# Kernel optimization log

Hardware: AMD Instinct MI355X
Metric: run time of the kernel (lower is better)

## Reference

```python
import jax, jax.numpy as jnp
import numpy as np

H = 2048          # hidden_size
I = 768           # moe_intermediate_size
E = 64            # num_experts
TOP_K = 8         # num_experts_per_tok (norm_topk_prob=True)
B, S = 1, 1024


def setup_inputs() -> dict:
    key = jax.random.key(0)
    ks = jax.random.split(key, 5)
    scale = 0.02
    return {
        "hidden_states": jax.random.normal(ks[0], (B, S, H), dtype=jnp.float32),
        "W_router": jax.random.normal(ks[1], (H, E), dtype=jnp.float32) * scale,
        "W_gate": jax.random.normal(ks[2], (E, H, I), dtype=jnp.float32) * scale,
        "W_up": jax.random.normal(ks[3], (E, H, I), dtype=jnp.float32) * scale,
        "W_down": jax.random.normal(ks[4], (E, I, H), dtype=jnp.float32) * scale,
    }


def reference(hidden_states, W_router, W_gate, W_up, W_down):
    b, s, h = hidden_states.shape
    x = hidden_states.reshape(-1, h)                      # [T, H]

    # --- Qwen3MoeTopKRouter: linear gate -> fp32 softmax -> top-k -> renorm ---
    logits = x @ W_router                                 # [T, E]
    probs = jax.nn.softmax(logits.astype(jnp.float32), axis=-1)
    top_w, top_idx = jax.lax.top_k(probs, TOP_K)          # [T, K]
    top_w = top_w / jnp.sum(top_w, axis=-1, keepdims=True)  # norm_topk_prob
    top_w = top_w.astype(x.dtype)

    # combine weights per (token, expert): zero if expert not selected
    comb = jnp.sum(jax.nn.one_hot(top_idx, E, dtype=x.dtype) * top_w[..., None], axis=1)  # [T, E]

    # --- per-expert SwiGLU MLP: down(silu(gate(x)) * up(x)), dense-masked ---
    g = jnp.einsum('th,ehi->eti', x, W_gate)              # [E, T, I]
    u = jnp.einsum('th,ehi->eti', x, W_up)                # [E, T, I]
    hmid = jax.nn.silu(g) * u                             # [E, T, I]
    # fold combine weight into the intermediate to avoid an [E, T, H] buffer
    hmid = hmid * comb.T[:, :, None]                      # [E, T, I]
    out = jnp.einsum('eti,eih->th', hmid, W_down)         # [T, H]

    return out.reshape(b, s, h)
```

## Files before the change

### kernel.cpp

```cpp
#include <hip/hip_runtime.h>
#include <hip/hip_bf16.h>

#define H_DIM 2048
#define I_DIM 768
#define NEXP 64
#define TOPK 8
#define NTOK 1024
#define BM 256
#define BKS 32

typedef float f32x4 __attribute__((ext_vector_type(4)));
typedef unsigned int u32x4 __attribute__((ext_vector_type(4)));
typedef unsigned int u32x2 __attribute__((ext_vector_type(2)));
typedef short bf16v8 __attribute__((ext_vector_type(8)));
typedef unsigned short u16x8 __attribute__((ext_vector_type(8)));
typedef unsigned int u32;

#define NTLOAD __builtin_nontemporal_load

#define WS_NEEDED 50954752ull

__device__ inline unsigned short f2bf(float f) {
    union { float f; u32 u; } v; v.f = f;
    u32 r = (v.u + 0x7FFFu + ((v.u >> 16) & 1u)) >> 16;
    return (unsigned short)r;
}
__device__ inline u32 pack2(float a, float b) {
    return (u32)f2bf(a) | ((u32)f2bf(b) << 16);
}

__global__ void zero_kernel(float4* p, int n4) {
    int i = blockIdx.x * blockDim.x + threadIdx.x;
    if (i < n4) p[i] = (float4){0.f, 0.f, 0.f, 0.f};
}

__global__ void xconv_kernel(const float4* __restrict__ x, ushort4* __restrict__ xbf, int n4) {
    int i = blockIdx.x * blockDim.x + threadIdx.x;
    if (i < n4) {
        float4 v = x[i];
        ushort4 o;
        o.x = f2bf(v.x); o.y = f2bf(v.y); o.z = f2bf(v.z); o.w = f2bf(v.w);
        xbf[i] = o;
    }
}

__global__ __launch_bounds__(256) void router_kernel(
    const float* __restrict__ x, const float* __restrict__ Wr,
    int* __restrict__ topk_idx, float* __restrict__ topk_w)
{
    const int t   = blockIdx.x;
    const int tid = threadIdx.x;
    const int lane = tid & 63;
    const int wv   = tid >> 6;
    __shared__ float xs[H_DIM];
    __shared__ float red[4][64];

    const float* xrow = x + (size_t)t * H_DIM;
    {
        const float4* src = (const float4*)xrow;
        float4* dst = (float4*)xs;
        dst[tid]       = src[tid];
        dst[tid + 256] = src[tid + 256];
    }
    __syncthreads();

    float acc = 0.f;
    const int h0 = wv * 512;
    #pragma unroll 8
    for (int h = h0; h < h0 + 512; ++h) acc += xs[h] * Wr[(size_t)h * NEXP + lane];
    red[wv][lane] = acc;
    __syncthreads();

    if (tid < 64) {
        const int e = tid;
        float logit = red[0][e] + red[1][e] + red[2][e] + red[3][e];

        float m = logit;
        #pragma unroll
        for (int o = 32; o > 0; o >>= 1) m = fmaxf(m, __shfl_xor(m, o));
        float p = __expf(logit - m);
        float s = p;
        #pragma unroll
        for (int o = 32; o > 0; o >>= 1) s += __shfl_xor(s, o);
        float prob = p / s;

        float myp = prob;
        float kw[TOPK]; int kid[TOPK]; float wsum = 0.f;
        #pragma unroll
        for (int k = 0; k < TOPK; ++k) {
            float v = myp; int bi = e;
            #pragma unroll
            for (int o = 32; o > 0; o >>= 1) {
                float ov = __shfl_xor(v, o);
                int   oi = __shfl_xor(bi, o);
                if (ov > v || (ov == v && oi < bi)) { v = ov; bi = oi; }
            }
            kw[k] = v; kid[k] = bi; wsum += v;
            if (e == bi) myp = -1.f;
        }
        if (e == 0) {
            float inv = 1.f / wsum;
            #pragma unroll
            for (int k = 0; k < TOPK; ++k) {
                topk_idx[t * TOPK + k] = kid[k];
                topk_w[t * TOPK + k]   = kw[k] * inv;
            }
        }
    }
}

__global__ __launch_bounds__(64) void listbuild_kernel(
    const int* __restrict__ topk_idx, const float* __restrict__ topk_w,
    int* __restrict__ counts, int* __restrict__ lists, float* __restrict__ wlist,
    int* __restrict__ invmap)
{
    const int e = blockIdx.x;
    const int lane = threadIdx.x;
    int n = 0;
    for (int base = 0; base < NTOK * TOPK; base += 64) {
        int s = base + lane;
        int idx = topk_idx[s];
        bool match = (idx == e);
        unsigned long long mask = __ballot(match);
        int pre = __popcll(mask & ((1ull << lane) - 1ull));
        if (match) {
            lists[e * NTOK + n + pre] = s >> 3;
            wlist[e * NTOK + n + pre] = topk_w[s];
            invmap[s] = n + pre;
        }
        n += __popcll(mask);
    }
    if (lane == 0) counts[e] = n;
}

__global__ __launch_bounds__(64) void scan_kernel(
    const int* __restrict__ counts, int* __restrict__ offsets)
{
    int e = threadIdx.x;
    int v = counts[e];
    int xacc = v;
    #pragma unroll
    for (int o = 1; o < 64; o <<= 1) {
        int y = __shfl_up(xacc, o);
        if (e >= o) xacc += y;
    }
    offsets[e] = xacc - v;
}

#define MFMA_BF16 __builtin_amdgcn_mfma_f32_16x16x32_bf16
#define LGKM0()  asm volatile("s_waitcnt lgkmcnt(0)" ::: "memory")
#define RAWBAR() __builtin_amdgcn_s_barrier()

__global__ __launch_bounds__(512) void gateup_kernel(
    const unsigned short* __restrict__ xbf,
    const float* __restrict__ Wg, const float* __restrict__ Wu,
    const int* __restrict__ counts, const int* __restrict__ offsets,
    const int* __restrict__ lists, const float* __restrict__ wlist,
    unsigned short* __restrict__ hmid)
{
    const int b  = blockIdx.x;
    const int wg = (b & 7) * 192 + (b >> 3);
    const int itile = wg % 24;
    const int e     = wg / 24;

    const int count = counts[e];
    if (count == 0) return;
    const int off = offsets[e];
    const int i0 = itile * 32;

    __shared__ unsigned short Alds[2][BM][40];
    __shared__ u32 Bgl[2][32 * 20];
    __shared__ u32 Bul[2][32 * 20];

    const int tid  = threadIdx.x;
    const int lane = tid & 63;
    const int wid  = tid >> 6;
    const int wm   = wid >> 1, wn = wid & 1;
    const int kb   = lane >> 4;
    const int l15  = lane & 15;

    const int ar = tid >> 1;
    const int ah = (tid & 1) * 16;
    const int bnn  = tid & 31;
    const int bkq  = (tid >> 5) & 7;
    const int bmat = tid >> 8;
    const float* WB = (bmat ? Wu : Wg) + (size_t)e * H_DIM * I_DIM + i0 + bnn;
    const int key4w = 4 * ((bnn >> 3) & 3);
    const int bwoff = bnn * 20 + ((2 * bkq) ^ key4w);
    const int brn   = wn * 16 + l15;
    const int key4r = 4 * ((brn >> 3) & 3);

    for (int mstart = 0; mstart < count; mstart += BM) {
        const int pr = mstart + ar;
        const bool aact = pr < count;
        const unsigned short* xrow = xbf + (size_t)(aact ? lists[e * NTOK + pr] : 0) * H_DIM + ah;
        const bool mact = (mstart + wm * 64) < count;

        f32x4 accg[4], accu[4];
        #pragma unroll
        for (int i = 0; i < 4; ++i) {
            accg[i] = (f32x4){0.f, 0.f, 0.f, 0.f};
            accu[i] = (f32x4){0.f, 0.f, 0.f, 0.f};
        }

        u32x4 aA0, aA1, aB0, aB1;
        float bA0, bA1, bA2, bA3;
        float bB0, bB1, bB2, bB3;

#define GU_LOADA(P0,P1,h)                                                       \
        if (aact) {                                                             \
            const u32x4* pa_ = (const u32x4*)(xrow + (h));                      \
            P0 = pa_[0]; P1 = pa_[1];                                           \
        }
#define GU_LOADB(R0,R1,R2,R3,h)                                                 \
        {                                                                       \
            R0 = NTLOAD(WB + (size_t)((h) + 4 * bkq)     * I_DIM);              \
            R1 = NTLOAD(WB + (size_t)((h) + 4 * bkq + 1) * I_DIM);              \
            R2 = NTLOAD(WB + (size_t)((h) + 4 * bkq + 2) * I_DIM);              \
            R3 = NTLOAD(WB + (size_t)((h) + 4 * bkq + 3) * I_DIM);              \
        }
#define GU_STORE(BUF,P0,P1,R0,R1,R2,R3)                                         \
        if (aact) {                                                             \
            *(u32x4*)&Alds[BUF][ar][ah]     = P0;                               \
            *(u32x4*)&Alds[BUF][ar][ah + 8] = P1;                               \
        }                                                                       \
        {                                                                       \
            u32x2 w_; w_.x = pack2(R0, R1); w_.y = pack2(R2, R3);               \
            *(u32x2*)((bmat ? Bul[BUF] : Bgl[BUF]) + bwoff) = w_;               \
        }
#define GU_MFMA(BUF)                                                            \
        if (mact) {                                                             \
            bf16v8 af[4], bg, bu;                                               \
            _Pragma("unroll")                                                   \
            for (int mf = 0; mf < 4; ++mf)                                      \
                af[mf] = *(const bf16v8*)&Alds[BUF][wm * 64 + mf * 16 + l15][kb * 8]; \
            bg = *(const bf16v8*)&Bgl[BUF][brn * 20 + ((4 * kb) ^ key4r)];      \
            bu = *(const bf16v8*)&Bul[BUF][brn * 20 + ((4 * kb) ^ key4r)];      \
            _Pragma("unroll")                                                   \
            for (int mf = 0; mf < 4; ++mf) {                                    \
                accg[mf] = MFMA_BF16(af[mf], bg, accg[mf], 0, 0, 0);            \
                accu[mf] = MFMA_BF16(af[mf], bu, accu[mf], 0, 0, 0);            \
            }                                                                   \
        }
#define GU_PHASE(BUF,P0,P1,R0,R1,R2,R3,nh)                                      \
        GU_STORE(BUF, P0, P1, R0, R1, R2, R3);                                  \
        if ((nh) < H_DIM) { GU_LOADB(R0, R1, R2, R3, (nh)); GU_LOADA(P0, P1, (nh)); } \
        LGKM0();                                                                \
        RAWBAR();                                                               \
        __builtin_amdgcn_s_setprio(1);                                          \
        GU_MFMA(BUF);                                                           \
        __builtin_amdgcn_s_setprio(0);

        GU_LOADB(bA0, bA1, bA2, bA3, 0);    GU_LOADA(aA0, aA1, 0);
        GU_LOADB(bB0, bB1, bB2, bB3, BKS);  GU_LOADA(aB0, aB1, BKS);

        for (int hh = 0; hh < H_DIM; hh += 2 * BKS) {
            GU_PHASE(0, aA0, aA1, bA0, bA1, bA2, bA3, hh + 2 * BKS);
            GU_PHASE(1, aB0, aB1, bB0, bB1, bB2, bB3, hh + 3 * BKS);
        }
        __syncthreads();
#undef GU_LOADA
#undef GU_LOADB
#undef GU_STORE
#undef GU_MFMA
#undef GU_PHASE

        if (mact) {
            #pragma unroll
            for (int mf = 0; mf < 4; ++mf)
                #pragma unroll
                for (int r = 0; r < 4; ++r) {
                    int pos = mstart + wm * 64 + mf * 16 + kb * 4 + r;
                    if (pos < count) {
                        float wgt = wlist[e * NTOK + pos];
                        float g = accg[mf][r], u = accu[mf][r];
                        float s = 1.f / (1.f + __expf(-g));
                        hmid[(size_t)(off + pos) * I_DIM + i0 + wn * 16 + l15] = f2bf(g * s * u * wgt);
                    }
                }
        }
    }
}

template <bool USE_PART>
__global__ __launch_bounds__(512) void down_kernel(
    const unsigned short* __restrict__ hmid, const float* __restrict__ Wd,
    const int* __restrict__ counts, const int* __restrict__ offsets,
    const int* __restrict__ lists, float* __restrict__ out,
    unsigned short* __restrict__ part)
{
    const int b  = blockIdx.x;
    const int wg = (b & 7) * 512 + (b >> 3);
    const int htile = wg % 64;
    const int e     = wg / 64;

    const int count = counts[e];
    if (count == 0) return;
    const int off = offsets[e];
    const int h0 = htile * 32;

    __shared__ unsigned short Alds[2][BM][40];
    __shared__ u32 Bdl[2][32 * 20];

    const int tid  = threadIdx.x;
    const int lane = tid & 63;
    const int wid  = tid >> 6;
    const int wm   = wid >> 1, wn = wid & 1;
    const int kb   = lane >> 4;
    const int l15  = lane & 15;

    const int ar = tid >> 1;
    const int ah = (tid & 1) * 16;
    const int bnn  = tid & 31;
    const int bkq  = (tid >> 5) & 7;
    const bool bact = tid < 256;
    const float* WB = Wd + (size_t)e * I_DIM * H_DIM + h0 + bnn;
    const int key4w = 4 * ((bnn >> 3) & 3);
    const int bwoff = bnn * 20 + ((2 * bkq) ^ key4w);
    const int brn   = wn * 16 + l15;
    const int key4r = 4 * ((brn >> 3) & 3);

    for (int mstart = 0; mstart < count; mstart += BM) {
        const int pr = mstart + ar;
        const bool aact = pr < count;
        const unsigned short* hrow = hmid + (size_t)(off + (aact ? pr : 0)) * I_DIM + ah;
        const bool mact = (mstart + wm * 64) < count;

        f32x4 acc[4];
        #pragma unroll
        for (int i = 0; i < 4; ++i) acc[i] = (f32x4){0.f, 0.f, 0.f, 0.f};

        u32x4 aA0, aA1, aB0, aB1;
        float bA0, bA1, bA2, bA3;
        float bB0, bB1, bB2, bB3;

#define DN_LOADA(P0,P1,k)                                                       \
        if (aact) {                                                             \
            const u32x4* p_ = (const u32x4*)(hrow + (k));                       \
            P0 = p_[0]; P1 = p_[1];                                             \
        }
#define DN_LOADB(R0,R1,R2,R3,k)                                                 \
        if (bact) {                                                             \
            R0 = NTLOAD(WB + (size_t)((k) + 4 * bkq)     * H_DIM);              \
            R1 = NTLOAD(WB + (size_t)((k) + 4 * bkq + 1) * H_DIM);              \
            R2 = NTLOAD(WB + (size_t)((k) + 4 * bkq + 2) * H_DIM);              \
            R3 = NTLOAD(WB + (size_t)((k) + 4 * bkq + 3) * H_DIM);              \
        }
#define DN_STORE(BUF,P0,P1,R0,R1,R2,R3)                                         \
        if (aact) {                                                             \
            *(u32x4*)&Alds[BUF][ar][ah]     = P0;                               \
            *(u32x4*)&Alds[BUF][ar][ah + 8] = P1;                               \
        }                                                                       \
        if (bact) {                                                             \
            u32x2 w_; w_.x = pack2(R0, R1); w_.y = pack2(R2, R3);               \
            *(u32x2*)(Bdl[BUF] + bwoff) = w_;                                   \
        }
#define DN_MFMA(BUF)                                                            \
        if (mact) {                                                             \
            bf16v8 af[4], bd;                                                   \
            _Pragma("unroll")                                                   \
            for (int mf = 0; mf < 4; ++mf)                                      \
                af[mf] = *(const bf16v8*)&Alds[BUF][wm * 64 + mf * 16 + l15][kb * 8]; \
            bd = *(const bf16v8*)&Bdl[BUF][brn * 20 + ((4 * kb) ^ key4r)];      \
            _Pragma("unroll")                                                   \
            for (int mf = 0; mf < 4; ++mf)                                      \
                acc[mf] = MFMA_BF16(af[mf], bd, acc[mf], 0, 0, 0);              \
        }
#define DN_PHASE(BUF,P0,P1,R0,R1,R2,R3,nk)                                      \
        DN_STORE(BUF, P0, P1, R0, R1, R2, R3);                                  \
        if ((nk) < I_DIM) { DN_LOADB(R0, R1, R2, R3, (nk)); DN_LOADA(P0, P1, (nk)); } \
        LGKM0();                                                                \
        RAWBAR();                                                               \
        __builtin_amdgcn_s_setprio(1);                                          \
        DN_MFMA(BUF);                                                           \
        __builtin_amdgcn_s_setprio(0);

        DN_LOADB(bA0, bA1, bA2, bA3, 0);    DN_LOADA(aA0, aA1, 0);
        DN_LOADB(bB0, bB1, bB2, bB3, BKS);  DN_LOADA(aB0, aB1, BKS);

        for (int ii = 0; ii < I_DIM; ii += 2 * BKS) {
            DN_PHASE(0, aA0, aA1, bA0, bA1, bA2, bA3, ii + 2 * BKS);
            DN_PHASE(1, aB0, aB1, bB0, bB1, bB2, bB3, ii + 3 * BKS);
        }
        __syncthreads();
#undef DN_LOADA
#undef DN_LOADB
#undef DN_STORE
#undef DN_MFMA
#undef DN_PHASE

        if (mact) {
            #pragma unroll
            for (int mf = 0; mf < 4; ++mf)
                #pragma unroll
                for (int r = 0; r < 4; ++r) {
                    int pos = mstart + wm * 64 + mf * 16 + kb * 4 + r;
                    if (pos < count) {
                        if constexpr (USE_PART) {
                            part[(size_t)(off + pos) * H_DIM + h0 + wn * 16 + l15] =
                                f2bf(acc[mf][r]);
                        } else {
                            int tok = lists[e * NTOK + pos];
                            atomicAdd(&out[(size_t)tok * H_DIM + h0 + wn * 16 + l15],
                                      acc[mf][r]);
                        }
                    }
                }
        }
    }
}

__global__ __launch_bounds__(256) void reduce_kernel(
    const unsigned short* __restrict__ part,
    const int* __restrict__ topk_idx, const int* __restrict__ invmap,
    const int* __restrict__ offsets, float* __restrict__ out)
{
    const int t   = blockIdx.x;
    const int tid = threadIdx.x;
    __shared__ int slots[TOPK];
    if (tid < TOPK) {
        int s = t * TOPK + tid;
        slots[tid] = offsets[topk_idx[s]] + invmap[s];
    }
    __syncthreads();

    const int c = tid * 8;
    float acc[8] = {0.f, 0.f, 0.f, 0.f, 0.f, 0.f, 0.f, 0.f};
    #pragma unroll
    for (int k = 0; k < TOPK; ++k) {
        u16x8 v = *(const u16x8*)&part[(size_t)slots[k] * H_DIM + c];
        #pragma unroll
        for (int j = 0; j < 8; ++j)
            acc[j] += __uint_as_float((u32)(unsigned short)v[j] << 16);
    }
    float4* dst = (float4*)&out[(size_t)t * H_DIM + c];
    dst[0] = (float4){acc[0], acc[1], acc[2], acc[3]};
    dst[1] = (float4){acc[4], acc[5], acc[6], acc[7]};
}

extern "C" void kernel_launch(void* const* d_in, const int* in_sizes, int n_in,
                              void* d_out, int out_size, void* d_ws, size_t ws_size,
                              hipStream_t stream) {
    const float* x  = (const float*)d_in[0];
    const float* Wr = (const float*)d_in[1];
    const float* Wg = (const float*)d_in[2];
    const float* Wu = (const float*)d_in[3];
    const float* Wd = (const float*)d_in[4];
    float* out = (float*)d_out;

    char* ws = (char*)d_ws;
    int*   topk_idx = (int*)  (ws + 0);
    float* topk_w   = (float*)(ws + 32768);
    int*   counts   = (int*)  (ws + 65536);
    int*   offsets  = (int*)  (ws + 65792);
    int*   lists    = (int*)  (ws + 66048);
    float* wlist    = (float*)(ws + 328192);
    int*   invmap   = (int*)  (ws + 590336);
    unsigned short* hmid = (unsigned short*)(ws + 623104);
    unsigned short* xbf  = (unsigned short*)(ws + 13206016);
    unsigned short* part = (unsigned short*)(ws + 17400320);

    const bool usePart = ws_size >= WS_NEEDED;

    hipLaunchKernelGGL(xconv_kernel, dim3((NTOK * H_DIM / 4 + 255) / 256), dim3(256), 0, stream,
                       (const float4*)x, (ushort4*)xbf, NTOK * H_DIM / 4);
    hipLaunchKernelGGL(router_kernel, dim3(NTOK), dim3(256), 0, stream,
                       x, Wr, topk_idx, topk_w);
    hipLaunchKernelGGL(listbuild_kernel, dim3(NEXP), dim3(64), 0, stream,
                       topk_idx, topk_w, counts, lists, wlist, invmap);
    hipLaunchKernelGGL(scan_kernel, dim3(1), dim3(64), 0, stream,
                       counts, offsets);
    hipLaunchKernelGGL(gateup_kernel, dim3(24 * NEXP), dim3(512), 0, stream,
                       xbf, Wg, Wu, counts, offsets, lists, wlist, hmid);
    if (usePart) {
        hipLaunchKernelGGL((down_kernel<true>), dim3(64 * NEXP), dim3(512), 0, stream,
                           hmid, Wd, counts, offsets, lists, out, part);
        hipLaunchKernelGGL(reduce_kernel, dim3(NTOK), dim3(256), 0, stream,
                           part, topk_idx, invmap, offsets, out);
    } else {
        const int nout4 = NTOK * H_DIM / 4;
        hipLaunchKernelGGL(zero_kernel, dim3((nout4 + 255) / 256), dim3(256), 0, stream,
                           (float4*)out, nout4);
        hipLaunchKernelGGL((down_kernel<false>), dim3(64 * NEXP), dim3(512), 0, stream,
                           hmid, Wd, counts, offsets, lists, out, part);
    }
}
```

Baseline: 476.4 us.

## Split expert M dimension across blocks with 128-row tiles and drop nontemporal loads

Halves the M tile to 128 rows and 256 threads, and gives each 128-row chunk of an expert's token list its own block instead of looping over chunks inside one block. This doubles the grid for both the gate/up and down GEMMs, which is meant to improve load balance and occupancy across CUs. The weight loads change from nontemporal to plain loads, so weights can stay in cache when several chunks of the same expert read them. The cost is that weight tiles are now fetched once per chunk, roughly twice for experts with more than 128 tokens, and each thread does more B loads.

```diff
diff --git a/kernel.cpp b/kernel.cpp
--- a/kernel.cpp
+++ b/kernel.cpp
@@ -6,7 +6,7 @@
 #define NEXP 64
 #define TOPK 8
 #define NTOK 1024
-#define BM 256
+#define BM 128
 #define BKS 32
 
 typedef float f32x4 __attribute__((ext_vector_type(4)));
@@ -15,8 +15,6 @@
 typedef short bf16v8 __attribute__((ext_vector_type(8)));
 typedef unsigned short u16x8 __attribute__((ext_vector_type(8)));
 typedef unsigned int u32;
-
-#define NTLOAD __builtin_nontemporal_load
 
 #define WS_NEEDED 50954752ull
 
@@ -151,7 +149,7 @@
 #define LGKM0()  asm volatile("s_waitcnt lgkmcnt(0)" ::: "memory")
 #define RAWBAR() __builtin_amdgcn_s_barrier()
 
-__global__ __launch_bounds__(512) void gateup_kernel(
+__global__ __launch_bounds__(256) void gateup_kernel(
     const unsigned short* __restrict__ xbf,
     const float* __restrict__ Wg, const float* __restrict__ Wu,
     const int* __restrict__ counts, const int* __restrict__ offsets,
@@ -159,12 +157,15 @@
     unsigned short* __restrict__ hmid)
 {
     const int b  = blockIdx.x;
-    const int wg = (b & 7) * 192 + (b >> 3);
-    const int itile = wg % 24;
-    const int e     = wg / 24;
+    const int wg = (b & 7) * 384 + (b >> 3);
+    const int e      = wg / 48;
+    const int rem    = wg % 48;
+    const int itile  = rem >> 1;
+    const int mchunk = rem & 1;
 
     const int count = counts[e];
-    if (count == 0) return;
+    const int mstart = mchunk * BM;
+    if (mstart >= count) return;
     const int off = offsets[e];
     const int i0 = itile * 32;
 
@@ -181,121 +182,123 @@
 
     const int ar = tid >> 1;
     const int ah = (tid & 1) * 16;
-    const int bnn  = tid & 31;
-    const int bkq  = (tid >> 5) & 7;
-    const int bmat = tid >> 8;
-    const float* WB = (bmat ? Wu : Wg) + (size_t)e * H_DIM * I_DIM + i0 + bnn;
+    const int bnn = tid & 31;
+    const int bkq = tid >> 5;
+    const float* WBg = Wg + (size_t)e * H_DIM * I_DIM + i0 + bnn;
+    const float* WBu = Wu + (size_t)e * H_DIM * I_DIM + i0 + bnn;
     const int key4w = 4 * ((bnn >> 3) & 3);
     const int bwoff = bnn * 20 + ((2 * bkq) ^ key4w);
     const int brn   = wn * 16 + l15;
     const int key4r = 4 * ((brn >> 3) & 3);
 
-    for (int mstart = 0; mstart < count; mstart += BM) {
-        const int pr = mstart + ar;
-        const bool aact = pr < count;
-        const unsigned short* xrow = xbf + (size_t)(aact ? lists[e * NTOK + pr] : 0) * H_DIM + ah;
-        const bool mact = (mstart + wm * 64) < count;
-
-        f32x4 accg[4], accu[4];
-        #pragma unroll
-        for (int i = 0; i < 4; ++i) {
-            accg[i] = (f32x4){0.f, 0.f, 0.f, 0.f};
-            accu[i] = (f32x4){0.f, 0.f, 0.f, 0.f};
-        }
-
-        u32x4 aA0, aA1, aB0, aB1;
-        float bA0, bA1, bA2, bA3;
-        float bB0, bB1, bB2, bB3;
+    const int pr = mstart + ar;
+    const bool aact = pr < count;
+    const unsigned short* xrow = xbf + (size_t)(aact ? lists[e * NTOK + pr] : 0) * H_DIM + ah;
+    const bool mact = (mstart + wm * 64) < count;
+
+    f32x4 accg[4], accu[4];
+    #pragma unroll
+    for (int i = 0; i < 4; ++i) {
+        accg[i] = (f32x4){0.f, 0.f, 0.f, 0.f};
+        accu[i] = (f32x4){0.f, 0.f, 0.f, 0.f};
+    }
+
+    u32x4 aA0, aA1, aB0, aB1;
+    float gA0, gA1, gA2, gA3, uA0, uA1, uA2, uA3;
+    float gB0, gB1, gB2, gB3, uB0, uB1, uB2, uB3;
 
 #define GU_LOADA(P0,P1,h)                                                       \
-        if (aact) {                                                             \
-            const u32x4* pa_ = (const u32x4*)(xrow + (h));                      \
-            P0 = pa_[0]; P1 = pa_[1];                                           \
-        }
-#define GU_LOADB(R0,R1,R2,R3,h)                                                 \
-        {                                                                       \
-            R0 = NTLOAD(WB + (size_t)((h) + 4 * bkq)     * I_DIM);              \
-            R1 = NTLOAD(WB + (size_t)((h) + 4 * bkq + 1) * I_DIM);              \
-            R2 = NTLOAD(WB + (size_t)((h) + 4 * bkq + 2) * I_DIM);              \
-            R3 = NTLOAD(WB + (size_t)((h) + 4 * bkq + 3) * I_DIM);              \
-        }
-#define GU_STORE(BUF,P0,P1,R0,R1,R2,R3)                                         \
-        if (aact) {                                                             \
-            *(u32x4*)&Alds[BUF][ar][ah]     = P0;                               \
-            *(u32x4*)&Alds[BUF][ar][ah + 8] = P1;                               \
+    if (aact) {                                                                 \
+        const u32x4* pa_ = (const u32x4*)(xrow + (h));                          \
+        P0 = pa_[0]; P1 = pa_[1];                                               \
+    }
+#define GU_LOADB(G0,G1,G2,G3,U0,U1,U2,U3,h)                                     \
+    {                                                                           \
+        const float* pg_ = WBg + (size_t)((h) + 4 * bkq) * I_DIM;               \
+        const float* pu_ = WBu + (size_t)((h) + 4 * bkq) * I_DIM;               \
+        G0 = pg_[0]; G1 = pg_[I_DIM]; G2 = pg_[2 * I_DIM]; G3 = pg_[3 * I_DIM]; \
+        U0 = pu_[0]; U1 = pu_[I_DIM]; U2 = pu_[2 * I_DIM]; U3 = pu_[3 * I_DIM]; \
+    }
+#define GU_STORE(BUF,P0,P1,G0,G1,G2,G3,U0,U1,U2,U3)                             \
+    if (aact) {                                                                 \
+        *(u32x4*)&Alds[BUF][ar][ah]     = P0;                                   \
+        *(u32x4*)&Alds[BUF][ar][ah + 8] = P1;                                   \
+    }                                                                           \
+    {                                                                           \
+        u32x2 wg_; wg_.x = pack2(G0, G1); wg_.y = pack2(G2, G3);                \
+        *(u32x2*)(Bgl[BUF] + bwoff) = wg_;                                      \
+        u32x2 wu_; wu_.x = pack2(U0, U1); wu_.y = pack2(U2, U3);                \
+        *(u32x2*)(Bul[BUF] + bwoff) = wu_;                                      \
+    }
+#define GU_MFMA(BUF)                                                            \
+    if (mact) {                                                                 \
+        bf16v8 af[4], bg, bu;                                                   \
+        _Pragma("unroll")                                                       \
+        for (int mf = 0; mf < 4; ++mf)                                          \
+            af[mf] = *(const bf16v8*)&Alds[BUF][wm * 64 + mf * 16 + l15][kb * 8]; \
+        bg = *(const bf16v8*)&Bgl[BUF][brn * 20 + ((4 * kb) ^ key4r)];          \
+        bu = *(const bf16v8*)&Bul[BUF][brn * 20 + ((4 * kb) ^ key4r)];          \
+        _Pragma("unroll")                                                       \
+        for (int mf = 0; mf < 4; ++mf) {                                        \
+            accg[mf] = MFMA_BF16(af[mf], bg, accg[mf], 0, 0, 0);                \
+            accu[mf] = MFMA_BF16(af[mf], bu, accu[mf], 0, 0, 0);                \
         }                                                                       \
-        {                                                                       \
-            u32x2 w_; w_.x = pack2(R0, R1); w_.y = pack2(R2, R3);               \
-            *(u32x2*)((bmat ? Bul[BUF] : Bgl[BUF]) + bwoff) = w_;               \
-        }
-#define GU_MFMA(BUF)                                                            \
-        if (mact) {                                                             \
-            bf16v8 af[4], bg, bu;                                               \
-            _Pragma("unroll")                                                   \
-            for (int mf = 0; mf < 4; ++mf)                                      \
-                af[mf] = *(const bf16v8*)&Alds[BUF][wm * 64 + mf * 16 + l15][kb * 8]; \
-            bg = *(const bf16v8*)&Bgl[BUF][brn * 20 + ((4 * kb) ^ key4r)];      \
-            bu = *(const bf16v8*)&Bul[BUF][brn * 20 + ((4 * kb) ^ key4r)];      \
-            _Pragma("unroll")                                                   \
-            for (int mf = 0; mf < 4; ++mf) {                                    \
-                accg[mf] = MFMA_BF16(af[mf], bg, accg[mf], 0, 0, 0);            \
-                accu[mf] = MFMA_BF16(af[mf], bu, accu[mf], 0, 0, 0);            \
-            }                                                                   \
-        }
-#define GU_PHASE(BUF,P0,P1,R0,R1,R2,R3,nh)                                      \
-        GU_STORE(BUF, P0, P1, R0, R1, R2, R3);                                  \
-        if ((nh) < H_DIM) { GU_LOADB(R0, R1, R2, R3, (nh)); GU_LOADA(P0, P1, (nh)); } \
-        LGKM0();                                                                \
-        RAWBAR();                                                               \
-        __builtin_amdgcn_s_setprio(1);                                          \
-        GU_MFMA(BUF);                                                           \
-        __builtin_amdgcn_s_setprio(0);
-
-        GU_LOADB(bA0, bA1, bA2, bA3, 0);    GU_LOADA(aA0, aA1, 0);
-        GU_LOADB(bB0, bB1, bB2, bB3, BKS);  GU_LOADA(aB0, aB1, BKS);
-
-        for (int hh = 0; hh < H_DIM; hh += 2 * BKS) {
-            GU_PHASE(0, aA0, aA1, bA0, bA1, bA2, bA3, hh + 2 * BKS);
-            GU_PHASE(1, aB0, aB1, bB0, bB1, bB2, bB3, hh + 3 * BKS);
-        }
-        __syncthreads();
+    }
+#define GU_PHASE(BUF,P0,P1,G0,G1,G2,G3,U0,U1,U2,U3,nh)                          \
+    GU_STORE(BUF, P0, P1, G0, G1, G2, G3, U0, U1, U2, U3);                      \
+    if ((nh) < H_DIM) { GU_LOADB(G0,G1,G2,G3,U0,U1,U2,U3,(nh)); GU_LOADA(P0,P1,(nh)); } \
+    LGKM0();                                                                    \
+    RAWBAR();                                                                   \
+    __builtin_amdgcn_s_setprio(1);                                              \
+    GU_MFMA(BUF);                                                               \
+    __builtin_amdgcn_s_setprio(0);
+
+    GU_LOADB(gA0,gA1,gA2,gA3,uA0,uA1,uA2,uA3, 0);    GU_LOADA(aA0, aA1, 0);
+    GU_LOADB(gB0,gB1,gB2,gB3,uB0,uB1,uB2,uB3, BKS);  GU_LOADA(aB0, aB1, BKS);
+
+    for (int hh = 0; hh < H_DIM; hh += 2 * BKS) {
+        GU_PHASE(0, aA0, aA1, gA0,gA1,gA2,gA3,uA0,uA1,uA2,uA3, hh + 2 * BKS);
+        GU_PHASE(1, aB0, aB1, gB0,gB1,gB2,gB3,uB0,uB1,uB2,uB3, hh + 3 * BKS);
+    }
 #undef GU_LOADA
 #undef GU_LOADB
 #undef GU_STORE
 #undef GU_MFMA
 #undef GU_PHASE
 
-        if (mact) {
+    if (mact) {
+        #pragma unroll
+        for (int mf = 0; mf < 4; ++mf)
             #pragma unroll
-            for (int mf = 0; mf < 4; ++mf)
-                #pragma unroll
-                for (int r = 0; r < 4; ++r) {
-                    int pos = mstart + wm * 64 + mf * 16 + kb * 4 + r;
-                    if (pos < count) {
-                        float wgt = wlist[e * NTOK + pos];
-                        float g = accg[mf][r], u = accu[mf][r];
-                        float s = 1.f / (1.f + __expf(-g));
-                        hmid[(size_t)(off + pos) * I_DIM + i0 + wn * 16 + l15] = f2bf(g * s * u * wgt);
-                    }
+            for (int r = 0; r < 4; ++r) {
+                int pos = mstart + wm * 64 + mf * 16 + kb * 4 + r;
+                if (pos < count) {
+                    float wgt = wlist[e * NTOK + pos];
+                    float g = accg[mf][r], u = accu[mf][r];
+                    float s = 1.f / (1.f + __expf(-g));
+                    hmid[(size_t)(off + pos) * I_DIM + i0 + wn * 16 + l15] = f2bf(g * s * u * wgt);
                 }
-        }
+            }
     }
 }
 
 template <bool USE_PART>
-__global__ __launch_bounds__(512) void down_kernel(
+__global__ __launch_bounds__(256) void down_kernel(
     const unsigned short* __restrict__ hmid, const float* __restrict__ Wd,
     const int* __restrict__ counts, const int* __restrict__ offsets,
     const int* __restrict__ lists, float* __restrict__ out,
     unsigned short* __restrict__ part)
 {
     const int b  = blockIdx.x;
-    const int wg = (b & 7) * 512 + (b >> 3);
-    const int htile = wg % 64;
-    const int e     = wg / 64;
+    const int wg = (b & 7) * 1024 + (b >> 3);
+    const int e      = wg / 128;
+    const int rem    = wg % 128;
+    const int htile  = rem >> 1;
+    const int mchunk = rem & 1;
 
     const int count = counts[e];
-    if (count == 0) return;
+    const int mstart = mchunk * BM;
+    if (mstart >= count) return;
     const int off = offsets[e];
     const int h0 = htile * 32;
 
@@ -311,102 +314,96 @@
 
     const int ar = tid >> 1;
     const int ah = (tid & 1) * 16;
-    const int bnn  = tid & 31;
-    const int bkq  = (tid >> 5) & 7;
-    const bool bact = tid < 256;
+    const int bnn = tid & 31;
+    const int bkq = tid >> 5;
     const float* WB = Wd + (size_t)e * I_DIM * H_DIM + h0 + bnn;
     const int key4w = 4 * ((bnn >> 3) & 3);
     const int bwoff = bnn * 20 + ((2 * bkq) ^ key4w);
     const int brn   = wn * 16 + l15;
     const int key4r = 4 * ((brn >> 3) & 3);
 
-    for (int mstart = 0; mstart < count; mstart += BM) {
-        const int pr = mstart + ar;
-        const bool aact = pr < count;
-        const unsigned short* hrow = hmid + (size_t)(off + (aact ? pr : 0)) * I_DIM + ah;
-        const bool mact = (mstart + wm * 64) < count;
-
-        f32x4 acc[4];
-        #pragma unroll
-        for (int i = 0; i < 4; ++i) acc[i] = (f32x4){0.f, 0.f, 0.f, 0.f};
-
-        u32x4 aA0, aA1, aB0, aB1;
-        float bA0, bA1, bA2, bA3;
-        float bB0, bB1, bB2, bB3;
+    const int pr = mstart + ar;
+    const bool aact = pr < count;
+    const unsigned short* hrow = hmid + (size_t)(off + (aact ? pr : 0)) * I_DIM + ah;
+    const bool mact = (mstart + wm * 64) < count;
+
+    f32x4 acc[4];
+    #pragma unroll
+    for (int i = 0; i < 4; ++i) acc[i] = (f32x4){0.f, 0.f, 0.f, 0.f};
+
+    u32x4 aA0, aA1, aB0, aB1;
+    float dA0, dA1, dA2, dA3;
+    float dB0, dB1, dB2, dB3;
 
 #define DN_LOADA(P0,P1,k)                                                       \
-        if (aact) {                                                             \
-            const u32x4* p_ = (const u32x4*)(hrow + (k));                       \
-            P0 = p_[0]; P1 = p_[1];                                             \
-        }
+    if (aact) {                                                                 \
+        const u32x4* p_ = (const u32x4*)(hrow + (k));                           \
+        P0 = p_[0]; P1 = p_[1];                                                 \
+    }
 #define DN_LOADB(R0,R1,R2,R3,k)                                                 \
-        if (bact) {                                                             \
-            R0 = NTLOAD(WB + (size_t)((k) + 4 * bkq)     * H_DIM);              \
-            R1 = NTLOAD(WB + (size_t)((k) + 4 * bkq + 1) * H_DIM);              \
-            R2 = NTLOAD(WB + (size_t)((k) + 4 * bkq + 2) * H_DIM);              \
-            R3 = NTLOAD(WB + (size_t)((k) + 4 * bkq + 3) * H_DIM);              \
-        }
+    {                                                                           \
+        const float* pd_ = WB + (size_t)((k) + 4 * bkq) * H_DIM;                \
+        R0 = pd_[0]; R1 = pd_[H_DIM]; R2 = pd_[2 * H_DIM]; R3 = pd_[3 * H_DIM]; \
+    }
 #define DN_STORE(BUF,P0,P1,R0,R1,R2,R3)                                         \
-        if (aact) {                                                             \
-            *(u32x4*)&Alds[BUF][ar][ah]     = P0;                               \
-            *(u32x4*)&Alds[BUF][ar][ah + 8] = P1;                               \
-        }                                                                       \
-        if (bact) {                                                             \
-            u32x2 w_; w_.x = pack2(R0, R1); w_.y = pack2(R2, R3);               \
-            *(u32x2*)(Bdl[BUF] + bwoff) = w_;                                   \
-        }
+    if (aact) {                                                                 \
+        *(u32x4*)&Alds[BUF][ar][ah]     = P0;                                   \
+        *(u32x4*)&Alds[BUF][ar][ah + 8] = P1;                                   \
+    }                                                                           \
+    {                                                                           \
+        u32x2 w_; w_.x = pack2(R0, R1); w_.y = pack2(R2, R3);                   \
+        *(u32x2*)(Bdl[BUF] + bwoff) = w_;                                       \
+    }
 #define DN_MFMA(BUF)                                                            \
-        if (mact) {                                                             \
-            bf16v8 af[4], bd;                                                   \
-            _Pragma("unroll")                                                   \
-            for (int mf = 0; mf < 4; ++mf)                                      \
-                af[mf] = *(const bf16v8*)&Alds[BUF][wm * 64 + mf * 16 + l15][kb * 8]; \
-            bd = *(const bf16v8*)&Bdl[BUF][brn * 20 + ((4 * kb) ^ key4r)];      \
-            _Pragma("unroll")                                                   \
-            for (int mf = 0; mf < 4; ++mf)                                      \
-                acc[mf] = MFMA_BF16(af[mf], bd, acc[mf], 0, 0, 0);              \
-        }
+    if (mact) {                                                                 \
+        bf16v8 af[4], bd;                                                       \
+        _Pragma("unroll")                                                       \
+        for (int mf = 0; mf < 4; ++mf)                                          \
+            af[mf] = *(const bf16v8*)&Alds[BUF][wm * 64 + mf * 16 + l15][kb * 8]; \
+        bd = *(const bf16v8*)&Bdl[BUF][brn * 20 + ((4 * kb) ^ key4r)];          \
+        _Pragma("unroll")                                                       \
+        for (int mf = 0; mf < 4; ++mf)                                          \
+            acc[mf] = MFMA_BF16(af[mf], bd, acc[mf], 0, 0, 0);                  \
+    }
 #define DN_PHASE(BUF,P0,P1,R0,R1,R2,R3,nk)                                      \
-        DN_STORE(BUF, P0, P1, R0, R1, R2, R3);                                  \
-        if ((nk) < I_DIM) { DN_LOADB(R0, R1, R2, R3, (nk)); DN_LOADA(P0, P1, (nk)); } \
-        LGKM0();                                                                \
-        RAWBAR();                                                               \
-        __builtin_amdgcn_s_setprio(1);                                          \
-        DN_MFMA(BUF);                                                           \
-        __builtin_amdgcn_s_setprio(0);
-
-        DN_LOADB(bA0, bA1, bA2, bA3, 0);    DN_LOADA(aA0, aA1, 0);
-        DN_LOADB(bB0, bB1, bB2, bB3, BKS);  DN_LOADA(aB0, aB1, BKS);
-
-        for (int ii = 0; ii < I_DIM; ii += 2 * BKS) {
-            DN_PHASE(0, aA0, aA1, bA0, bA1, bA2, bA3, ii + 2 * BKS);
-            DN_PHASE(1, aB0, aB1, bB0, bB1, bB2, bB3, ii + 3 * BKS);
-        }
-        __syncthreads();
+    DN_STORE(BUF, P0, P1, R0, R1, R2, R3);                                      \
+    if ((nk) < I_DIM) { DN_LOADB(R0, R1, R2, R3, (nk)); DN_LOADA(P0, P1, (nk)); } \
+    LGKM0();                                                                    \
+    RAWBAR();                                                                   \
+    __builtin_amdgcn_s_setprio(1);                                              \
+    DN_MFMA(BUF);                                                               \
+    __builtin_amdgcn_s_setprio(0);
+
+    DN_LOADB(dA0, dA1, dA2, dA3, 0);    DN_LOADA(aA0, aA1, 0);
+    DN_LOADB(dB0, dB1, dB2, dB3, BKS);  DN_LOADA(aB0, aB1, BKS);
+
+    for (int ii = 0; ii < I_DIM; ii += 2 * BKS) {
+        DN_PHASE(0, aA0, aA1, dA0, dA1, dA2, dA3, ii + 2 * BKS);
+        DN_PHASE(1, aB0, aB1, dB0, dB1, dB2, dB3, ii + 3 * BKS);
+    }
 #undef DN_LOADA
 #undef DN_LOADB
 #undef DN_STORE
 #undef DN_MFMA
 #undef DN_PHASE
 
-        if (mact) {
+    if (mact) {
+        #pragma unroll
+        for (int mf = 0; mf < 4; ++mf)
             #pragma unroll
-            for (int mf = 0; mf < 4; ++mf)
-                #pragma unroll
-                for (int r = 0; r < 4; ++r) {
-                    int pos = mstart + wm * 64 + mf * 16 + kb * 4 + r;
-                    if (pos < count) {
-                        if constexpr (USE_PART) {
-                            part[(size_t)(off + pos) * H_DIM + h0 + wn * 16 + l15] =
-                                f2bf(acc[mf][r]);
-                        } else {
-                            int tok = lists[e * NTOK + pos];
-                            atomicAdd(&out[(size_t)tok * H_DIM + h0 + wn * 16 + l15],
-                                      acc[mf][r]);
-                        }
+            for (int r = 0; r < 4; ++r) {
+                int pos = mstart + wm * 64 + mf * 16 + kb * 4 + r;
+                if (pos < count) {
+                    if constexpr (USE_PART) {
+                        part[(size_t)(off + pos) * H_DIM + h0 + wn * 16 + l15] =
+                            f2bf(acc[mf][r]);
+                    } else {
+                        int tok = lists[e * NTOK + pos];
+                        atomicAdd(&out[(size_t)tok * H_DIM + h0 + wn * 16 + l15],
+                                  acc[mf][r]);
                     }
                 }
-        }
+            }
     }
 }
 
@@ -470,10 +467,10 @@
                        topk_idx, topk_w, counts, lists, wlist, invmap);
     hipLaunchKernelGGL(scan_kernel, dim3(1), dim3(64), 0, stream,
                        counts, offsets);
-    hipLaunchKernelGGL(gateup_kernel, dim3(24 * NEXP), dim3(512), 0, stream,
+    hipLaunchKernelGGL(gateup_kernel, dim3(48 * NEXP), dim3(256), 0, stream,
                        xbf, Wg, Wu, counts, offsets, lists, wlist, hmid);
     if (usePart) {
-        hipLaunchKernelGGL((down_kernel<true>), dim3(64 * NEXP), dim3(512), 0, stream,
+        hipLaunchKernelGGL((down_kernel<true>), dim3(128 * NEXP), dim3(256), 0, stream,
                            hmid, Wd, counts, offsets, lists, out, part);
         hipLaunchKernelGGL(reduce_kernel, dim3(NTOK), dim3(256), 0, stream,
                            part, topk_idx, invmap, offsets, out);
@@ -481,7 +478,7 @@
         const int nout4 = NTOK * H_DIM / 4;
         hipLaunchKernelGGL(zero_kernel, dim3((nout4 + 255) / 256), dim3(256), 0, stream,
                            (float4*)out, nout4);
-        hipLaunchKernelGGL((down_kernel<false>), dim3(64 * NEXP), dim3(512), 0, stream,
+        hipLaunchKernelGGL((down_kernel<false>), dim3(128 * NEXP), dim3(256), 0, stream,
                            hmid, Wd, counts, offsets, lists, out, part);
     }
 }
```

Measured after the change: 683.8 us. 43.6% more time.
